# Kernel tuning notes

Measured on AMD Instinct MI355X. Metric: run time of the kernel, lower is better.

Reference implementation:

```python
import jax, jax.numpy as jnp
import numpy as np

B = 8          # number of subgraphs (seq_start_end rows)
N = 2048       # nodes per subgraph (equal-size segments)
D = 64         # h_dim
H = 4          # gat_heads
ALPHA = 0.2    # leaky relu slope


def setup_inputs() -> dict:
    key = jax.random.key(0)
    k1, k2, k3, k4, k5 = jax.random.split(key, 5)
    h_states = jax.random.normal(k1, (B * N, D), dtype=jnp.float32)
    # xavier-ish scales
    W_heads = jax.random.normal(k2, (H, D, D), dtype=jnp.float32) * (1.414 * np.sqrt(2.0 / (D + D)))
    a_heads = jax.random.normal(k3, (H, 2 * D), dtype=jnp.float32) * (1.414 * np.sqrt(2.0 / (2 * D + 1)))
    W_out = jax.random.normal(k4, (H * D, D), dtype=jnp.float32) * (1.414 * np.sqrt(2.0 / (H * D + D)))
    a_out = jax.random.normal(k5, (2 * D,), dtype=jnp.float32) * (1.414 * np.sqrt(2.0 / (2 * D + 1)))
    starts = jnp.arange(B, dtype=jnp.int32) * N
    seq_start_end = jnp.stack([starts, starts + N], axis=1)  # (B, 2)
    return {"h_states": h_states, "W_heads": W_heads, "a_heads": a_heads,
            "W_out": W_out, "a_out": a_out, "seq_start_end": seq_start_end}


def _gat_layer(x, W, a):
    """Dense GAT layer. Equivalent to the torch.cat O(N^2*2d) construction,
    rewritten as separate a1/a2 projections + broadcast add. Eval mode (no dropout)."""
    h = x @ W                      # (N, dout)
    d = W.shape[1]
    s1 = h @ a[:d]                 # (N,)  score contribution of source node i
    s2 = h @ a[d:]                 # (N,)  score contribution of target node j
    e = jax.nn.leaky_relu(s1[:, None] + s2[None, :], ALPHA)  # (N, N)
    attn = jax.nn.softmax(e, axis=1)
    return attn @ h                # (N, dout)


def reference(h_states, W_heads, a_heads, W_out, a_out, seq_start_end):
    # seq_start_end encodes B equal contiguous segments of length N -> reshape
    x = h_states.reshape(B, N, D)

    def per_graph(xg):  # xg: (N, D)
        # multi-head attention layers, concat=True -> elu on each head output
        hp = jax.vmap(lambda W, a: jax.nn.elu(_gat_layer(xg, W, a)))(W_heads, a_heads)  # (H, N, D)
        xc = jnp.transpose(hp, (1, 0, 2)).reshape(N, H * D)
        # output attention layer, concat=False (no elu inside), then elu + log_softmax outside
        out = jax.nn.elu(_gat_layer(xc, W_out, a_out))   # (N, D)
        return jax.nn.log_softmax(out, axis=1)

    return jax.vmap(per_graph)(x).reshape(B * N, D)
```

## Files before the change

kernel.cpp:

```cpp
#include <hip/hip_runtime.h>
#include <math.h>

#define NTOT 16384
#define NSEG 2048
#define TROW 65
#define TSTRIDE 133120ull
#define CSTRIDE 8385ull

#define OFF_HH   0ull
#define OFF_XC   4194304ull
#define OFF_S1H  8388608ull
#define OFF_S2H  8454144ull
#define OFF_S1O  8519680ull
#define OFF_S2O  8536064ull
#define OFF_SVAL 8552448ull
#define OFF_WN   8617984ull
#define OFF_SIDX 8683520ull
#define OFF_CA   8749056ull
#define OFF_CS   9017376ull
#define OFF_A    9285696ull
#define OFF_S    13545536ull

__device__ inline unsigned long long pack_key(float v, int idx) {
    unsigned u = __float_as_uint(v);
    u = (u & 0x80000000u) ? ~u : (u | 0x80000000u);
    return ((unsigned long long)u << 32) | (unsigned)idx;
}
__device__ inline float unpack_key(unsigned long long k) {
    unsigned u = (unsigned)(k >> 32);
    u = (u & 0x80000000u) ? (u ^ 0x80000000u) : ~u;
    return __uint_as_float(u);
}
__device__ inline unsigned long long shfl_xor_u64(unsigned long long x, int mask) {
    unsigned lo = (unsigned)x, hi = (unsigned)(x >> 32);
    lo = (unsigned)__shfl_xor((int)lo, mask, 64);
    hi = (unsigned)__shfl_xor((int)hi, mask, 64);
    return ((unsigned long long)hi << 32) | lo;
}

__global__ __launch_bounds__(256) void gemm1_k(const float* __restrict__ X,
                                               const float* __restrict__ Wh,
                                               const float* __restrict__ aH,
                                               float* __restrict__ hh,
                                               float* __restrict__ s1h,
                                               float* __restrict__ s2h) {
    __shared__ float As[64][68];
    __shared__ float Bs[64][68];
    const int tid = threadIdx.x;
    const int bm = blockIdx.x, h = blockIdx.y;
    const int c0 = tid & 63, r0 = tid >> 6;
#pragma unroll
    for (int r = 0; r < 16; ++r) {
        int row = r0 + r * 4;
        As[c0][row] = X[(size_t)(bm * 64 + row) * 64 + c0];
        Bs[row][c0] = Wh[h * 4096 + row * 64 + c0];
    }
    __syncthreads();
    const int tx = tid & 15, ty = tid >> 4;
    const int m0 = ty * 4, n0 = tx * 4;
    float acc[4][4] = {};
#pragma unroll
    for (int kk = 0; kk < 64; ++kk) {
        float4 a = *(const float4*)&As[kk][m0];
        float4 b = *(const float4*)&Bs[kk][n0];
        acc[0][0] += a.x * b.x; acc[0][1] += a.x * b.y; acc[0][2] += a.x * b.z; acc[0][3] += a.x * b.w;
        acc[1][0] += a.y * b.x; acc[1][1] += a.y * b.y; acc[1][2] += a.y * b.z; acc[1][3] += a.y * b.w;
        acc[2][0] += a.z * b.x; acc[2][1] += a.z * b.y; acc[2][2] += a.z * b.z; acc[2][3] += a.z * b.w;
        acc[3][0] += a.w * b.x; acc[3][1] += a.w * b.y; acc[3][2] += a.w * b.z; acc[3][3] += a.w * b.w;
    }
#pragma unroll
    for (int i = 0; i < 4; ++i) {
        float4 v = make_float4(acc[i][0], acc[i][1], acc[i][2], acc[i][3]);
        *(float4*)&hh[(size_t)(bm * 64 + m0 + i) * 256 + h * 64 + n0] = v;
    }
#pragma unroll
    for (int i = 0; i < 4; ++i) {
        float p1 = 0.f, p2 = 0.f;
#pragma unroll
        for (int jj = 0; jj < 4; ++jj) {
            p1 += acc[i][jj] * aH[h * 128 + n0 + jj];
            p2 += acc[i][jj] * aH[h * 128 + 64 + n0 + jj];
        }
#pragma unroll
        for (int off = 8; off; off >>= 1) {
            p1 += __shfl_xor(p1, off, 16);
            p2 += __shfl_xor(p2, off, 16);
        }
        if (tx == 0) {
            s1h[h * NTOT + bm * 64 + m0 + i] = p1;
            s2h[h * NTOT + bm * 64 + m0 + i] = p2;
        }
    }
}

__global__ __launch_bounds__(256) void gemm2_k(const float* __restrict__ XC,
                                               const float* __restrict__ Wo,
                                               const float* __restrict__ aO,
                                               float* __restrict__ hc,
                                               float* __restrict__ s1o,
                                               float* __restrict__ s2o) {
    __shared__ float As[64][68];
    __shared__ float Bs[64][68];
    const int tid = threadIdx.x;
    const int bm = blockIdx.x;
    const int c0 = tid & 63, r0 = tid >> 6;
    const int tx = tid & 15, ty = tid >> 4;
    const int m0 = ty * 4, n0 = tx * 4;
    float acc[4][4] = {};
    for (int kt = 0; kt < 4; ++kt) {
#pragma unroll
        for (int r = 0; r < 16; ++r) {
            int row = r0 + r * 4;
            As[c0][row] = XC[(size_t)(bm * 64 + row) * 256 + kt * 64 + c0];
            Bs[row][c0] = Wo[(kt * 64 + row) * 64 + c0];
        }
        __syncthreads();
#pragma unroll
        for (int kk = 0; kk < 64; ++kk) {
            float4 a = *(const float4*)&As[kk][m0];
            float4 b = *(const float4*)&Bs[kk][n0];
            acc[0][0] += a.x * b.x; acc[0][1] += a.x * b.y; acc[0][2] += a.x * b.z; acc[0][3] += a.x * b.w;
            acc[1][0] += a.y * b.x; acc[1][1] += a.y * b.y; acc[1][2] += a.y * b.z; acc[1][3] += a.y * b.w;
            acc[2][0] += a.z * b.x; acc[2][1] += a.z * b.y; acc[2][2] += a.z * b.z; acc[2][3] += a.z * b.w;
            acc[3][0] += a.w * b.x; acc[3][1] += a.w * b.y; acc[3][2] += a.w * b.z; acc[3][3] += a.w * b.w;
        }
        __syncthreads();
    }
#pragma unroll
    for (int i = 0; i < 4; ++i) {
        float4 v = make_float4(acc[i][0], acc[i][1], acc[i][2], acc[i][3]);
        *(float4*)&hc[(size_t)(bm * 64 + m0 + i) * 64 + n0] = v;
    }
#pragma unroll
    for (int i = 0; i < 4; ++i) {
        float p1 = 0.f, p2 = 0.f;
#pragma unroll
        for (int jj = 0; jj < 4; ++jj) {
            p1 += acc[i][jj] * aO[n0 + jj];
            p2 += acc[i][jj] * aO[64 + n0 + jj];
        }
#pragma unroll
        for (int off = 8; off; off >>= 1) {
            p1 += __shfl_xor(p1, off, 16);
            p2 += __shfl_xor(p2, off, 16);
        }
        if (tx == 0) {
            s1o[bm * 64 + m0 + i] = p1;
            s2o[bm * 64 + m0 + i] = p2;
        }
    }
}

__global__ __launch_bounds__(1024) void sort_k(const float* __restrict__ s2_all,
                                               int heads,
                                               float* __restrict__ g_sval,
                                               int* __restrict__ g_sidx,
                                               float* __restrict__ g_wN) {
    __shared__ unsigned long long sA[2][1024];
    __shared__ unsigned long long sB[2][1024];
    __shared__ float sM2;
    const int tid = threadIdx.x, t = blockIdx.x;
    const int g = t / heads, h = t % heads;
    const float* s2p = s2_all + (size_t)h * NTOT + (size_t)g * NSEG;

    unsigned long long a0 = pack_key(s2p[tid], tid);
    unsigned long long a1 = pack_key(s2p[tid + 1024], tid + 1024);
    int p = 0;
    for (int k = 2; k <= 2048; k <<= 1) {
        const bool up0 = (tid & k) == 0;
        const bool up1 = (((tid + 1024) & k) == 0);
        for (int j = k >> 1; j > 0; j >>= 1) {
            if (j >= 1024) {
                unsigned long long lo = a0 < a1 ? a0 : a1;
                unsigned long long hi = a0 < a1 ? a1 : a0;
                a0 = up0 ? lo : hi;
                a1 = up0 ? hi : lo;
            } else if (j >= 64) {
                sA[p][tid] = a0; sB[p][tid] = a1;
                __syncthreads();
                unsigned long long q0 = sA[p][tid ^ j], q1 = sB[p][tid ^ j];
                bool lower = (tid & j) == 0;
                a0 = ((a0 < q0) == (lower == up0)) ? a0 : q0;
                a1 = ((a1 < q1) == (lower == up1)) ? a1 : q1;
                p ^= 1;
            } else {
                unsigned long long q0 = shfl_xor_u64(a0, j);
                unsigned long long q1 = shfl_xor_u64(a1, j);
                bool lower = (tid & j) == 0;
                a0 = ((a0 < q0) == (lower == up0)) ? a0 : q0;
                a1 = ((a1 < q1) == (lower == up1)) ? a1 : q1;
            }
        }
    }
    float v0 = unpack_key(a0), v1 = unpack_key(a1);
    if (tid == 1023) sM2 = v1;
    __syncthreads();
    const float M2 = sM2;
    int i0 = (int)(unsigned)(a0 & 0xffffffffu);
    int i1 = (int)(unsigned)(a1 & 0xffffffffu);
    float w0 = __expf(0.2f * (v0 - M2));
    float w1 = __expf(0.2f * (v1 - M2));
    size_t o = (size_t)t * NSEG;
    g_sval[o + tid] = v0; g_sval[o + tid + 1024] = v1;
    g_sidx[o + tid] = i0; g_sidx[o + tid + 1024] = i1;
    g_wN[o + tid] = w0;   g_wN[o + tid + 1024] = w1;
}

__global__ __launch_bounds__(256) void tabw_k(const float* __restrict__ V,
                                              int heads, int vstride,
                                              const int* __restrict__ g_sidx,
                                              const float* __restrict__ g_wN,
                                              float* __restrict__ g_A, float* __restrict__ g_S,
                                              float* __restrict__ g_TA, float* __restrict__ g_TS) {
    const int t = blockIdx.y, g = t / heads, h = t % heads;
    const int wv = threadIdx.x >> 6, lane = threadIdx.x & 63;
    const int c = blockIdx.x * 4 + wv;
    const int base = c * 16;
    const float* Vp = V + (size_t)g * NSEG * vstride + h * 64;
    const int* sidx = g_sidx + (size_t)t * NSEG + base;
    const float* wnp = g_wN + (size_t)t * NSEG + base;
    float wn[16], vv[16];
#pragma unroll
    for (int j = 0; j < 16; ++j) wn[j] = wnp[j];
#pragma unroll
    for (int j = 0; j < 16; ++j) vv[j] = Vp[(size_t)sidx[j] * vstride + lane];
    float* A = g_A + (size_t)t * TSTRIDE;
    float* S = g_S + (size_t)t * TSTRIDE;
    float accA = 0.f, scaA = 0.f;
#pragma unroll
    for (int j = 0; j < 16; ++j) {
        size_t pos = base + j;
        A[pos * TROW + lane] = accA;
        if (lane == 0) A[pos * TROW + 64] = scaA;
        accA += wn[j] * vv[j]; scaA += wn[j];
    }
    g_TA[((size_t)t * 128 + c) * TROW + lane] = accA;
    if (lane == 0) g_TA[((size_t)t * 128 + c) * TROW + 64] = scaA;
    float accS = 0.f, scaS = 0.f;
#pragma unroll
    for (int j = 15; j >= 0; --j) {
        float w = wn[j], w2 = w * w, wp = w2 * w2 * w;
        accS += wp * vv[j]; scaS += wp;
        size_t pos = base + j;
        S[pos * TROW + lane] = accS;
        if (lane == 0) S[pos * TROW + 64] = scaS;
    }
    g_TS[((size_t)t * 128 + c) * TROW + lane] = accS;
    if (lane == 0) g_TS[((size_t)t * 128 + c) * TROW + 64] = scaS;
}

__global__ __launch_bounds__(256) void scan_k(const float* __restrict__ g_TA,
                                              const float* __restrict__ g_TS,
                                              float* __restrict__ g_CA,
                                              float* __restrict__ g_CS) {
    const int t = blockIdx.x, tid = threadIdx.x;
    if (tid < 65) {
        const float* TA = g_TA + (size_t)t * 128 * TROW + tid;
        float* CA = g_CA + (size_t)t * CSTRIDE + tid;
        float run = 0.f;
#pragma unroll 4
        for (int c = 0; c < 128; ++c) { CA[c * TROW] = run; run += TA[c * TROW]; }
        CA[128 * TROW] = run;
    } else if (tid >= 128 && tid < 193) {
        const int d = tid - 128;
        const float* TS = g_TS + (size_t)t * 128 * TROW + d;
        float* CS = g_CS + (size_t)t * CSTRIDE + d;
        float run = 0.f;
#pragma unroll 4
        for (int c = 127; c >= 0; --c) { CS[c * TROW] = run; run += TS[c * TROW]; }
    }
}

template <int MODE>
__global__ __launch_bounds__(256) void query_k(const float* __restrict__ s1_all,
                                               float* __restrict__ out,
                                               int heads, int ostride,
                                               const float* __restrict__ g_sval,
                                               const float* __restrict__ g_A,
                                               const float* __restrict__ g_S,
                                               const float* __restrict__ g_CA,
                                               const float* __restrict__ g_CS) {
    __shared__ float sval[NSEG];
    const int tid = threadIdx.x;
    const int t = blockIdx.y, g = t / heads, h = t % heads;
    const float4* sv4 = (const float4*)(g_sval + (size_t)t * NSEG);
    for (int i = tid; i < NSEG / 4; i += 256) ((float4*)sval)[i] = sv4[i];
    __syncthreads();
    const float M2 = sval[NSEG - 1];
    const int lane = tid & 63, wv = tid >> 6;
    const int q0 = blockIdx.x * 64 + wv * 16;
    const float* s1p = s1_all + (size_t)h * NTOT + (size_t)g * NSEG;
    float* outp = out + (size_t)g * NSEG * ostride + h * 64;
    const float* A = g_A + (size_t)t * TSTRIDE;
    const float* S = g_S + (size_t)t * TSTRIDE;
    const float* CA = g_CA + (size_t)t * CSTRIDE;
    const float* CS = g_CS + (size_t)t * CSTRIDE;
    int myq = q0 + (lane & 15);
    float s1v = s1p[myq];
    float th = -s1v;
    int lo = 0, hi = NSEG;
    while (lo < hi) { int mid = (lo + hi) >> 1; if (sval[mid] <= th) lo = mid + 1; else hi = mid; }
    for (int j = 0; j < 16; ++j) {
        int k = __shfl(lo, j, 64);
        float s1q = __shfl(s1v, j, 64);
        float accA, scaA, accS, scaS;
        if (k < NSEG) {
            const int c = k >> 4;
            const float* rowA = A + (size_t)k * TROW;
            const float* rowS = S + (size_t)k * TROW;
            const float* rowCA = CA + (size_t)c * TROW;
            const float* rowCS = CS + (size_t)c * TROW;
            accA = rowA[lane] + rowCA[lane]; scaA = rowA[64] + rowCA[64];
            accS = rowS[lane] + rowCS[lane]; scaS = rowS[64] + rowCS[64];
        } else {
            accA = CA[128 * TROW + lane]; scaA = CA[128 * TROW + 64];
            accS = 0.f; scaS = 0.f;
        }
        float cc = __expf(-0.8f * fmaxf(s1q + M2, 0.f));
        float o = (accS + cc * accA) / (scaS + cc * scaA);
        o = o > 0.f ? o : expm1f(o);
        int q = q0 + j;
        if (MODE == 0) {
            outp[(size_t)q * ostride + lane] = o;
        } else {
            float m = o;
#pragma unroll
            for (int off = 32; off; off >>= 1) m = fmaxf(m, __shfl_xor(m, off, 64));
            float e = __expf(o - m);
#pragma unroll
            for (int off = 32; off; off >>= 1) e += __shfl_xor(e, off, 64);
            outp[(size_t)q * ostride + lane] = o - m - __logf(e);
        }
    }
}

extern "C" void kernel_launch(void* const* d_in, const int* in_sizes, int n_in,
                              void* d_out, int out_size, void* d_ws, size_t ws_size,
                              hipStream_t stream) {
    const float* h_states = (const float*)d_in[0];
    const float* W_heads = (const float*)d_in[1];
    const float* a_heads = (const float*)d_in[2];
    const float* W_out = (const float*)d_in[3];
    const float* a_out = (const float*)d_in[4];
    float* w = (float*)d_ws;
    float* hh = w + OFF_HH;
    float* xc = w + OFF_XC;
    float* hc = w + OFF_HH;
    float* s1h = w + OFF_S1H;
    float* s2h = w + OFF_S2H;
    float* s1o = w + OFF_S1O;
    float* s2o = w + OFF_S2O;
    float* g_sval = w + OFF_SVAL;
    float* g_wN = w + OFF_WN;
    int* g_sidx = (int*)(w + OFF_SIDX);
    float* g_TA = w + OFF_XC;
    float* g_TS = w + OFF_XC + 266240;
    float* g_CA = w + OFF_CA;
    float* g_CS = w + OFF_CS;
    float* g_A = w + OFF_A;
    float* g_S = w + OFF_S;
    float* outp = (float*)d_out;

    gemm1_k<<<dim3(256, 4), 256, 0, stream>>>(h_states, W_heads, a_heads, hh, s1h, s2h);
    sort_k<<<32, 1024, 0, stream>>>(s2h, 4, g_sval, g_sidx, g_wN);
    tabw_k<<<dim3(32, 32), 256, 0, stream>>>(hh, 4, 256, g_sidx, g_wN, g_A, g_S, g_TA, g_TS);
    scan_k<<<32, 256, 0, stream>>>(g_TA, g_TS, g_CA, g_CS);
    query_k<0><<<dim3(32, 32), 256, 0, stream>>>(s1h, xc, 4, 256, g_sval, g_A, g_S, g_CA, g_CS);
    gemm2_k<<<256, 256, 0, stream>>>(xc, W_out, a_out, hc, s1o, s2o);
    sort_k<<<8, 1024, 0, stream>>>(s2o, 1, g_sval, g_sidx, g_wN);
    tabw_k<<<dim3(32, 8), 256, 0, stream>>>(hc, 1, 64, g_sidx, g_wN, g_A, g_S, g_TA, g_TS);
    scan_k<<<8, 256, 0, stream>>>(g_TA, g_TS, g_CA, g_CS);
    query_k<1><<<dim3(32, 8), 256, 0, stream>>>(s1o, outp, 1, 64, g_sval, g_A, g_S, g_CA, g_CS);
}
```

Baseline: 200.3 us.

## Fuse chunk scan into table kernel via last-block atomic; retile gemm2 and use nontemporal I/O

The separate scan kernel is folded into tabw_k: each block bumps a per-task atomic counter, and the last block to arrive computes the chunk prefix and suffix sums. This removes two kernel launches and their serialization gaps, at the cost of a memset and a tail block doing serial work. The second counter uses a threshold of 63 for the second pass, so it relies on the counters continuing to accumulate from the first pass without being reset. The change also halves the gemm2 tile to 32 rows to double its grid, switches table stores and loads to nontemporal hints, and fully unrolls the query loop.

```diff
diff --git a/kernel.cpp b/kernel.cpp
--- a/kernel.cpp
+++ b/kernel.cpp
@@ -20,6 +20,7 @@
 #define OFF_CS   9017376ull
 #define OFF_A    9285696ull
 #define OFF_S    13545536ull
+#define OFF_CNT  17805376ull
 
 __device__ inline unsigned long long pack_key(float v, int idx) {
     unsigned u = __float_as_uint(v);
@@ -99,40 +100,42 @@
                                                float* __restrict__ hc,
                                                float* __restrict__ s1o,
                                                float* __restrict__ s2o) {
-    __shared__ float As[64][68];
+    __shared__ float As[64][34];
     __shared__ float Bs[64][68];
     const int tid = threadIdx.x;
     const int bm = blockIdx.x;
     const int c0 = tid & 63, r0 = tid >> 6;
     const int tx = tid & 15, ty = tid >> 4;
-    const int m0 = ty * 4, n0 = tx * 4;
-    float acc[4][4] = {};
+    const int m0 = ty * 2, n0 = tx * 4;
+    float acc[2][4] = {};
     for (int kt = 0; kt < 4; ++kt) {
+#pragma unroll
+        for (int r = 0; r < 8; ++r) {
+            int row = r0 + r * 4;
+            As[c0][row] = XC[(size_t)(bm * 32 + row) * 256 + kt * 64 + c0];
+        }
 #pragma unroll
         for (int r = 0; r < 16; ++r) {
             int row = r0 + r * 4;
-            As[c0][row] = XC[(size_t)(bm * 64 + row) * 256 + kt * 64 + c0];
             Bs[row][c0] = Wo[(kt * 64 + row) * 64 + c0];
         }
         __syncthreads();
 #pragma unroll
         for (int kk = 0; kk < 64; ++kk) {
-            float4 a = *(const float4*)&As[kk][m0];
+            float2 a = *(const float2*)&As[kk][m0];
             float4 b = *(const float4*)&Bs[kk][n0];
             acc[0][0] += a.x * b.x; acc[0][1] += a.x * b.y; acc[0][2] += a.x * b.z; acc[0][3] += a.x * b.w;
             acc[1][0] += a.y * b.x; acc[1][1] += a.y * b.y; acc[1][2] += a.y * b.z; acc[1][3] += a.y * b.w;
-            acc[2][0] += a.z * b.x; acc[2][1] += a.z * b.y; acc[2][2] += a.z * b.z; acc[2][3] += a.z * b.w;
-            acc[3][0] += a.w * b.x; acc[3][1] += a.w * b.y; acc[3][2] += a.w * b.z; acc[3][3] += a.w * b.w;
         }
         __syncthreads();
     }
 #pragma unroll
-    for (int i = 0; i < 4; ++i) {
+    for (int i = 0; i < 2; ++i) {
         float4 v = make_float4(acc[i][0], acc[i][1], acc[i][2], acc[i][3]);
-        *(float4*)&hc[(size_t)(bm * 64 + m0 + i) * 64 + n0] = v;
-    }
-#pragma unroll
-    for (int i = 0; i < 4; ++i) {
+        *(float4*)&hc[(size_t)(bm * 32 + m0 + i) * 64 + n0] = v;
+    }
+#pragma unroll
+    for (int i = 0; i < 2; ++i) {
         float p1 = 0.f, p2 = 0.f;
 #pragma unroll
         for (int jj = 0; jj < 4; ++jj) {
@@ -145,8 +148,8 @@
             p2 += __shfl_xor(p2, off, 16);
         }
         if (tx == 0) {
-            s1o[bm * 64 + m0 + i] = p1;
-            s2o[bm * 64 + m0 + i] = p2;
+            s1o[bm * 32 + m0 + i] = p1;
+            s2o[bm * 32 + m0 + i] = p2;
         }
     }
 }
@@ -207,11 +210,14 @@
 }
 
 __global__ __launch_bounds__(256) void tabw_k(const float* __restrict__ V,
-                                              int heads, int vstride,
+                                              int heads, int vstride, int lastv,
                                               const int* __restrict__ g_sidx,
                                               const float* __restrict__ g_wN,
                                               float* __restrict__ g_A, float* __restrict__ g_S,
-                                              float* __restrict__ g_TA, float* __restrict__ g_TS) {
+                                              float* __restrict__ g_TA, float* __restrict__ g_TS,
+                                              float* __restrict__ g_CA, float* __restrict__ g_CS,
+                                              int* __restrict__ g_cnt) {
+    __shared__ int s_last;
     const int t = blockIdx.y, g = t / heads, h = t % heads;
     const int wv = threadIdx.x >> 6, lane = threadIdx.x & 63;
     const int c = blockIdx.x * 4 + wv;
@@ -230,8 +236,8 @@
 #pragma unroll
     for (int j = 0; j < 16; ++j) {
         size_t pos = base + j;
-        A[pos * TROW + lane] = accA;
-        if (lane == 0) A[pos * TROW + 64] = scaA;
+        __builtin_nontemporal_store(accA, &A[pos * TROW + lane]);
+        if (lane == 0) __builtin_nontemporal_store(scaA, &A[pos * TROW + 64]);
         accA += wn[j] * vv[j]; scaA += wn[j];
     }
     g_TA[((size_t)t * 128 + c) * TROW + lane] = accA;
@@ -242,24 +248,27 @@
         float w = wn[j], w2 = w * w, wp = w2 * w2 * w;
         accS += wp * vv[j]; scaS += wp;
         size_t pos = base + j;
-        S[pos * TROW + lane] = accS;
-        if (lane == 0) S[pos * TROW + 64] = scaS;
+        __builtin_nontemporal_store(accS, &S[pos * TROW + lane]);
+        if (lane == 0) __builtin_nontemporal_store(scaS, &S[pos * TROW + 64]);
     }
     g_TS[((size_t)t * 128 + c) * TROW + lane] = accS;
     if (lane == 0) g_TS[((size_t)t * 128 + c) * TROW + 64] = scaS;
-}
-
-__global__ __launch_bounds__(256) void scan_k(const float* __restrict__ g_TA,
-                                              const float* __restrict__ g_TS,
-                                              float* __restrict__ g_CA,
-                                              float* __restrict__ g_CS) {
-    const int t = blockIdx.x, tid = threadIdx.x;
+
+    if (threadIdx.x == 0) {
+        __threadfence();
+        int old = atomicAdd(&g_cnt[t], 1);
+        s_last = (old == lastv) ? 1 : 0;
+    }
+    __syncthreads();
+    if (!s_last) return;
+    __threadfence();
+    const int tid = threadIdx.x;
     if (tid < 65) {
         const float* TA = g_TA + (size_t)t * 128 * TROW + tid;
         float* CA = g_CA + (size_t)t * CSTRIDE + tid;
         float run = 0.f;
 #pragma unroll 4
-        for (int c = 0; c < 128; ++c) { CA[c * TROW] = run; run += TA[c * TROW]; }
+        for (int cc = 0; cc < 128; ++cc) { CA[cc * TROW] = run; run += TA[cc * TROW]; }
         CA[128 * TROW] = run;
     } else if (tid >= 128 && tid < 193) {
         const int d = tid - 128;
@@ -267,7 +276,7 @@
         float* CS = g_CS + (size_t)t * CSTRIDE + d;
         float run = 0.f;
 #pragma unroll 4
-        for (int c = 127; c >= 0; --c) { CS[c * TROW] = run; run += TS[c * TROW]; }
+        for (int cc = 127; cc >= 0; --cc) { CS[cc * TROW] = run; run += TS[cc * TROW]; }
     }
 }
 
@@ -300,6 +309,7 @@
     float th = -s1v;
     int lo = 0, hi = NSEG;
     while (lo < hi) { int mid = (lo + hi) >> 1; if (sval[mid] <= th) lo = mid + 1; else hi = mid; }
+#pragma unroll
     for (int j = 0; j < 16; ++j) {
         int k = __shfl(lo, j, 64);
         float s1q = __shfl(s1v, j, 64);
@@ -310,8 +320,10 @@
             const float* rowS = S + (size_t)k * TROW;
             const float* rowCA = CA + (size_t)c * TROW;
             const float* rowCS = CS + (size_t)c * TROW;
-            accA = rowA[lane] + rowCA[lane]; scaA = rowA[64] + rowCA[64];
-            accS = rowS[lane] + rowCS[lane]; scaS = rowS[64] + rowCS[64];
+            accA = __builtin_nontemporal_load(&rowA[lane]) + rowCA[lane];
+            scaA = __builtin_nontemporal_load(&rowA[64]) + rowCA[64];
+            accS = __builtin_nontemporal_load(&rowS[lane]) + rowCS[lane];
+            scaS = __builtin_nontemporal_load(&rowS[64]) + rowCS[64];
         } else {
             accA = CA[128 * TROW + lane]; scaA = CA[128 * TROW + 64];
             accS = 0.f; scaS = 0.f;
@@ -359,16 +371,16 @@
     float* g_CS = w + OFF_CS;
     float* g_A = w + OFF_A;
     float* g_S = w + OFF_S;
+    int* g_cnt = (int*)(w + OFF_CNT);
     float* outp = (float*)d_out;
 
+    hipMemsetAsync(g_cnt, 0, 32 * sizeof(int), stream);
     gemm1_k<<<dim3(256, 4), 256, 0, stream>>>(h_states, W_heads, a_heads, hh, s1h, s2h);
     sort_k<<<32, 1024, 0, stream>>>(s2h, 4, g_sval, g_sidx, g_wN);
-    tabw_k<<<dim3(32, 32), 256, 0, stream>>>(hh, 4, 256, g_sidx, g_wN, g_A, g_S, g_TA, g_TS);
-    scan_k<<<32, 256, 0, stream>>>(g_TA, g_TS, g_CA, g_CS);
+    tabw_k<<<dim3(32, 32), 256, 0, stream>>>(hh, 4, 256, 31, g_sidx, g_wN, g_A, g_S, g_TA, g_TS, g_CA, g_CS, g_cnt);
     query_k<0><<<dim3(32, 32), 256, 0, stream>>>(s1h, xc, 4, 256, g_sval, g_A, g_S, g_CA, g_CS);
-    gemm2_k<<<256, 256, 0, stream>>>(xc, W_out, a_out, hc, s1o, s2o);
+    gemm2_k<<<512, 256, 0, stream>>>(xc, W_out, a_out, hc, s1o, s2o);
     sort_k<<<8, 1024, 0, stream>>>(s2o, 1, g_sval, g_sidx, g_wN);
-    tabw_k<<<dim3(32, 8), 256, 0, stream>>>(hc, 1, 64, g_sidx, g_wN, g_A, g_S, g_TA, g_TS);
-    scan_k<<<8, 256, 0, stream>>>(g_TA, g_TS, g_CA, g_CS);
+    tabw_k<<<dim3(32, 8), 256, 0, stream>>>(hc, 1, 64, 63, g_sidx, g_wN, g_A, g_S, g_TA, g_TS, g_CA, g_CS, g_cnt);
     query_k<1><<<dim3(32, 8), 256, 0, stream>>>(s1o, outp, 1, 64, g_sval, g_A, g_S, g_CA, g_CS);
 }
```

Result: slower. 286.7 us (+43.1%).
